# Kernel optimization log

Hardware: AMD Instinct MI355X
Metric: run time of the kernel (lower is better)

## Reference

```python
import jax, jax.numpy as jnp
import numpy as np

EPS = 1e-7
IOU_THRESHOLD = 0.5
PENALTY_FACTOR = 0.1
BOX_LOSS_WEIGHT = 5.0
OBJ_LOSS_WEIGHT = 1.0
SMALL_OBJ_SCALE = 2.0
SMALL_SIZE_THRESHOLD = 0.05


def _xywh_to_xyxy(b):
    return jnp.concatenate([b[..., :2] - b[..., 2:] / 2, b[..., :2] + b[..., 2:] / 2], axis=-1)


def _bbox_ciou(box1, box2, eps=EPS):
    # box1, box2: (..., 4) in xyxy format
    b1_x1, b1_y1, b1_x2, b1_y2 = box1[..., 0], box1[..., 1], box1[..., 2], box1[..., 3]
    b2_x1, b2_y1, b2_x2, b2_y2 = box2[..., 0], box2[..., 1], box2[..., 2], box2[..., 3]
    b1_area = (b1_x2 - b1_x1) * (b1_y2 - b1_y1)
    b2_area = (b2_x2 - b2_x1) * (b2_y2 - b2_y1)
    inter_w = jnp.clip(jnp.minimum(b1_x2, b2_x2) - jnp.maximum(b1_x1, b2_x1), 0)
    inter_h = jnp.clip(jnp.minimum(b1_y2, b2_y2) - jnp.maximum(b1_y1, b2_y1), 0)
    inter_area = inter_w * inter_h
    union_area = b1_area + b2_area - inter_area + eps
    iou = inter_area / union_area
    c2 = (jnp.maximum(b1_x2, b2_x2) - jnp.minimum(b1_x1, b2_x1)) ** 2 + \
         (jnp.maximum(b1_y2, b2_y2) - jnp.minimum(b1_y1, b2_y1)) ** 2 + eps
    center_dist2 = ((b1_x1 + b1_x2) / 2 - (b2_x1 + b2_x2) / 2) ** 2 + \
                   ((b1_y1 + b1_y2) / 2 - (b2_y1 + b2_y2) / 2) ** 2
    w1, h1 = b1_x2 - b1_x1, b1_y2 - b1_y1
    w2, h2 = b2_x2 - b2_x1, b2_y2 - b2_y1
    v = (4.0 / (jnp.pi ** 2)) * (jnp.arctan(w1 / (h1 + eps)) - jnp.arctan(w2 / (h2 + eps))) ** 2
    alpha = v / (1 - iou + v + eps)
    return iou - (center_dist2 / c2 + alpha * v)


def setup_inputs() -> dict:
    key = jax.random.key(0)
    k0, k1, k2, k3, k4 = jax.random.split(key, 5)
    B, Np, Ng, C = 16, 8192, 128, 80
    return {
        "batch_y_hat": jax.random.uniform(k0, (B, Np, 4), dtype=jnp.float32),
        "batch_y": jax.random.uniform(k1, (B, Ng, 4), dtype=jnp.float32),
        "batch_obj_scores": jax.random.normal(k2, (B, Np), dtype=jnp.float32),
        "batch_class_pred": jax.random.normal(k3, (B, Np, C), dtype=jnp.float32),
        "batch_class_target": jax.random.randint(k4, (B, Ng), 0, C),
        "min_obj_score": 0,
    }


def reference(batch_y_hat, batch_y, batch_obj_scores, batch_class_pred, batch_class_target, min_obj_score):
    valid = batch_obj_scores > min_obj_score                      # (B, Np) kept predictions
    p = _xywh_to_xyxy(batch_y_hat)                                # (B, Np, 4)
    g = _xywh_to_xyxy(batch_y)                                    # (B, Ng, 4)
    # pairwise IoU (xywh compute_iou, which has no eps)
    lt = jnp.maximum(p[:, :, None, :2], g[:, None, :, :2])       # (B, Np, Ng, 2)
    rb = jnp.minimum(p[:, :, None, 2:], g[:, None, :, 2:])
    wh = jnp.clip(rb - lt, 0)
    inter = wh[..., 0] * wh[..., 1]                               # (B, Np, Ng)
    area_p = (p[..., 2] - p[..., 0]) * (p[..., 3] - p[..., 1])
    area_g = (g[..., 2] - g[..., 0]) * (g[..., 3] - g[..., 1])
    iou_mat = inter / (area_p[:, :, None] + area_g[:, None, :] - inter)
    max_iou = jnp.max(iou_mat, axis=-1)                           # (B, Np)
    match_idx = jnp.argmax(iou_mat, axis=-1)                      # (B, Np)
    matched = valid & (max_iou > IOU_THRESHOLD)
    unmatched = valid & ~matched
    # CIoU localization loss over matched preds
    matched_gt_xyxy = jnp.take_along_axis(g, match_idx[..., None], axis=1)   # (B, Np, 4)
    ciou_loss = 1.0 - _bbox_ciou(p, matched_gt_xyxy)              # (B, Np)
    is_small = (batch_y[..., 2] < SMALL_SIZE_THRESHOLD) | (batch_y[..., 3] < SMALL_SIZE_THRESHOLD)  # (B, Ng)
    w_small = jnp.where(jnp.take_along_axis(is_small, match_idx, axis=1), SMALL_OBJ_SCALE, 1.0)
    n_match = jnp.sum(matched, axis=1)
    loc_loss = jnp.where(n_match > 0,
                         jnp.sum(ciou_loss * w_small * matched, axis=1) / jnp.maximum(n_match, 1),
                         0.0)
    # classification loss over matched preds
    logp = jax.nn.log_softmax(batch_class_pred, axis=-1)          # (B, Np, C)
    tgt = jnp.take_along_axis(batch_class_target, match_idx, axis=1)
    ce = -jnp.take_along_axis(logp, tgt[..., None], axis=-1)[..., 0]
    cls_loss = jnp.where(n_match > 0,
                         jnp.sum(ce * w_small * matched, axis=1) / jnp.maximum(n_match, 1),
                         0.0)
    # penalty on unmatched objectness scores
    penalty = PENALTY_FACTOR * jnp.sum(batch_obj_scores * unmatched, axis=1)
    # objectness BCE-with-logits over valid preds, FN reweighted x2
    s = batch_obj_scores
    lbl = matched.astype(s.dtype)
    bce = jnp.clip(s, 0) - s * lbl + jnp.log1p(jnp.exp(-jnp.abs(s)))
    w_obj = jnp.where(matched & (s < 0.5), 2.0, 1.0)
    n_valid = jnp.sum(valid, axis=1)
    obj_loss = jnp.where(n_valid > 0,
                         jnp.sum(bce * w_obj * valid, axis=1) / jnp.maximum(n_valid, 1),
                         0.0)
    per_batch = BOX_LOSS_WEIGHT * loc_loss + OBJ_LOSS_WEIGHT * obj_loss + penalty + cls_loss
    valid_b = n_valid > 0
    n_vb = jnp.sum(valid_b)
    return jnp.sum(jnp.where(valid_b, per_batch, 0.0)) / jnp.maximum(n_vb, 1)
```

## Files before the change

kernel.cpp:

```cpp
#include <hip/hip_runtime.h>
#include <math.h>

#define B_  16
#define NP_ 8192
#define NG_ 128
#define NC_ 80

#define EPS_       1e-7f
#define IOU_THR_   0.5f
#define PEN_       0.1f
#define BOXW_      5.0f
#define SMALLSC_   2.0f
#define SMALLTH_   0.05f


__global__ __launch_bounds__(256) void yolo_main(
    const float* __restrict__ y_hat,
    const float* __restrict__ ygt,
    const float* __restrict__ obj,
    const float* __restrict__ clsp,
    const int*   __restrict__ tgt,
    const int*   __restrict__ min_s,
    float* __restrict__ acc)
{
    __shared__ float gx1[NG_], gy1[NG_], gx2[NG_], gy2[NG_], garea[NG_], gws[NG_];
    __shared__ int   gtc[NG_];
    __shared__ float wred[4][6];

    const int b   = blockIdx.y;
    const int tid = threadIdx.x;
    const int p   = blockIdx.x * 256 + tid;

    if (tid < NG_) {
        float4 gb = *(const float4*)(ygt + ((size_t)b * NG_ + tid) * 4);
        float x1 = gb.x - gb.z * 0.5f, y1 = gb.y - gb.w * 0.5f;
        float x2 = gb.x + gb.z * 0.5f, y2 = gb.y + gb.w * 0.5f;
        gx1[tid] = x1; gy1[tid] = y1; gx2[tid] = x2; gy2[tid] = y2;
        garea[tid] = (x2 - x1) * (y2 - y1);
        gws[tid]   = ((gb.z < SMALLTH_) || (gb.w < SMALLTH_)) ? SMALLSC_ : 1.0f;
        gtc[tid]   = tgt[b * NG_ + tid];
    }
    __syncthreads();

    const float min_score = (float)min_s[0];

    float4 pb = *(const float4*)(y_hat + ((size_t)b * NP_ + p) * 4);
    float px1 = pb.x - pb.z * 0.5f, py1 = pb.y - pb.w * 0.5f;
    float px2 = pb.x + pb.z * 0.5f, py2 = pb.y + pb.w * 0.5f;
    float area_p = (px2 - px1) * (py2 - py1);

    float bi_inter = -1.0f, bi_union = 1.0f;
    int   bi = 0;
    #pragma unroll 8
    for (int j = 0; j < NG_; ++j) {
        float ltx = fmaxf(px1, gx1[j]);
        float lty = fmaxf(py1, gy1[j]);
        float rbx = fminf(px2, gx2[j]);
        float rby = fminf(py2, gy2[j]);
        float w = fmaxf(rbx - ltx, 0.0f);
        float h = fmaxf(rby - lty, 0.0f);
        float inter = w * h;
        float uni = area_p + garea[j] - inter;
        bool better = inter * bi_union > bi_inter * uni;
        bi_inter = better ? inter : bi_inter;
        bi_union = better ? uni   : bi_union;
        bi       = better ? j     : bi;
    }
    float max_iou = bi_inter / bi_union;

    float s = obj[(size_t)b * NP_ + p];
    bool valid     = s > min_score;
    bool matched   = valid && (max_iou > IOU_THR_);
    bool unmatched = valid && !matched;

    float f_loc = 0.f, f_ce = 0.f, f_pen = 0.f, f_bce = 0.f;
    float n_m = matched ? 1.f : 0.f;
    float n_v = valid   ? 1.f : 0.f;

    if (unmatched) f_pen = PEN_ * s;

    if (valid) {
        float lbl = matched ? 1.f : 0.f;
        float bce = fmaxf(s, 0.f) - s * lbl + log1pf(expf(-fabsf(s)));
        float w_obj = (matched && s < 0.5f) ? 2.f : 1.f;
        f_bce = bce * w_obj;
    }

    if (matched) {
        float wsm = gws[bi];
        float bx1 = gx1[bi], by1 = gy1[bi], bx2 = gx2[bi], by2 = gy2[bi];
        float b1a = (px2 - px1) * (py2 - py1);
        float b2a = (bx2 - bx1) * (by2 - by1);
        float iw = fmaxf(fminf(px2, bx2) - fmaxf(px1, bx1), 0.f);
        float ih = fmaxf(fminf(py2, by2) - fmaxf(py1, by1), 0.f);
        float inter = iw * ih;
        float uni = b1a + b2a - inter + EPS_;
        float iou = inter / uni;
        float cw = fmaxf(px2, bx2) - fminf(px1, bx1);
        float ch = fmaxf(py2, by2) - fminf(py1, by1);
        float c2 = cw * cw + ch * ch + EPS_;
        float dx = (px1 + px2) * 0.5f - (bx1 + bx2) * 0.5f;
        float dy = (py1 + py2) * 0.5f - (by1 + by2) * 0.5f;
        float rho2 = dx * dx + dy * dy;
        float w1 = px2 - px1, h1 = py2 - py1;
        float w2 = bx2 - bx1, h2 = by2 - by1;
        float dat = atanf(w1 / (h1 + EPS_)) - atanf(w2 / (h2 + EPS_));
        float v = (float)(4.0 / (M_PI * M_PI)) * dat * dat;
        float alpha = v / (1.f - iou + v + EPS_);
        float ciou = iou - (rho2 / c2 + alpha * v);
        f_loc = (1.f - ciou) * wsm;

        const float* row = clsp + ((size_t)b * NP_ + p) * NC_;
        float m = -INFINITY;
        #pragma unroll
        for (int k = 0; k < NC_ / 4; ++k) {
            float4 v4 = ((const float4*)row)[k];
            m = fmaxf(m, fmaxf(fmaxf(v4.x, v4.y), fmaxf(v4.z, v4.w)));
        }
        float se = 0.f;
        #pragma unroll
        for (int k = 0; k < NC_ / 4; ++k) {
            float4 v4 = ((const float4*)row)[k];
            se += expf(v4.x - m) + expf(v4.y - m) + expf(v4.z - m) + expf(v4.w - m);
        }
        int t = gtc[bi];
        float ce = -(row[t] - m - logf(se));
        f_ce = ce * wsm;
    }

    float vals[6] = { n_m, n_v, f_loc, f_ce, f_pen, f_bce };
    #pragma unroll
    for (int i = 0; i < 6; ++i) {
        float v = vals[i];
        #pragma unroll
        for (int off = 32; off > 0; off >>= 1)
            v += __shfl_down(v, off, 64);
        vals[i] = v;
    }
    int wave = tid >> 6, lane = tid & 63;
    if (lane == 0) {
        #pragma unroll
        for (int i = 0; i < 6; ++i) wred[wave][i] = vals[i];
    }
    __syncthreads();
    if (tid == 0) {
        #pragma unroll
        for (int i = 0; i < 6; ++i) {
            float v = wred[0][i] + wred[1][i] + wred[2][i] + wred[3][i];
            atomicAdd(&acc[b * 6 + i], v);
        }
    }
}

__global__ __launch_bounds__(64) void yolo_final(const float* __restrict__ acc,
                                                 float* __restrict__ out)
{
    int b = threadIdx.x;
    float pb = 0.f, cnt = 0.f;
    if (b < B_) {
        float nm   = acc[b * 6 + 0];
        float nv   = acc[b * 6 + 1];
        float sloc = acc[b * 6 + 2];
        float sce  = acc[b * 6 + 3];
        float spen = acc[b * 6 + 4];
        float sbce = acc[b * 6 + 5];
        float loc = nm > 0.f ? sloc / nm : 0.f;
        float ce  = nm > 0.f ? sce  / nm : 0.f;
        float ob  = nv > 0.f ? sbce / nv : 0.f;
        float per = BOXW_ * loc + ob + spen + ce;
        if (nv > 0.f) { pb = per; cnt = 1.f; }
    }
    #pragma unroll
    for (int off = 32; off > 0; off >>= 1) {
        pb  += __shfl_down(pb,  off, 64);
        cnt += __shfl_down(cnt, off, 64);
    }
    if (b == 0) out[0] = pb / fmaxf(cnt, 1.f);
}

extern "C" void kernel_launch(void* const* d_in, const int* in_sizes, int n_in,
                              void* d_out, int out_size, void* d_ws, size_t ws_size,
                              hipStream_t stream) {
    const float* y_hat = (const float*)d_in[0];
    const float* ygt   = (const float*)d_in[1];
    const float* obj   = (const float*)d_in[2];
    const float* clsp  = (const float*)d_in[3];
    const int*   tgt   = (const int*)d_in[4];
    const int*   mins  = (const int*)d_in[5];
    float* acc = (float*)d_ws;
    float* out = (float*)d_out;

    hipMemsetAsync(acc, 0, B_ * 6 * sizeof(float), stream);

    dim3 grid(NP_ / 256, B_);
    yolo_main<<<grid, 256, 0, stream>>>(y_hat, ygt, obj, clsp, tgt, mins, acc);
    yolo_final<<<1, 64, 0, stream>>>(acc, out);
}
```

Measured before the change: 115.2 us.

## Split GT matching across two thread halves and drop atomics for per-block partials

Each block now handles 128 predictions with 256 threads: each half scans 64 ground-truth boxes and the two argmax results are merged through shared memory. This doubles the grid and shortens the serial IoU loop per thread. Block sums go to a per-block partial buffer instead of atomics, which removes the memset, and the final kernel reduces those partials. GT boxes are stored as float4 in shared memory. The cost is an extra barrier, and half the threads sit idle during the loss tail.

```diff
diff --git a/kernel.cpp b/kernel.cpp
--- a/kernel.cpp
+++ b/kernel.cpp
@@ -5,6 +5,8 @@
 #define NP_ 8192
 #define NG_ 128
 #define NC_ 80
+#define PPB_ 128
+#define NBX_ (NP_ / PPB_)
 
 #define EPS_       1e-7f
 #define IOU_THR_   0.5f
@@ -21,21 +23,25 @@
     const float* __restrict__ clsp,
     const int*   __restrict__ tgt,
     const int*   __restrict__ min_s,
-    float* __restrict__ acc)
+    float* __restrict__ part)
 {
-    __shared__ float gx1[NG_], gy1[NG_], gx2[NG_], gy2[NG_], garea[NG_], gws[NG_];
-    __shared__ int   gtc[NG_];
-    __shared__ float wred[4][6];
-
-    const int b   = blockIdx.y;
-    const int tid = threadIdx.x;
-    const int p   = blockIdx.x * 256 + tid;
+    __shared__ float4 g4[NG_];
+    __shared__ float  garea[NG_], gws[NG_];
+    __shared__ int    gtc[NG_];
+    __shared__ float  mbuf[PPB_][4];
+    __shared__ float  wred[4][6];
+
+    const int b    = blockIdx.y;
+    const int tid  = threadIdx.x;
+    const int pl   = tid & (PPB_ - 1);
+    const int half = tid >> 7;
+    const int p    = blockIdx.x * PPB_ + pl;
 
     if (tid < NG_) {
         float4 gb = *(const float4*)(ygt + ((size_t)b * NG_ + tid) * 4);
         float x1 = gb.x - gb.z * 0.5f, y1 = gb.y - gb.w * 0.5f;
         float x2 = gb.x + gb.z * 0.5f, y2 = gb.y + gb.w * 0.5f;
-        gx1[tid] = x1; gy1[tid] = y1; gx2[tid] = x2; gy2[tid] = y2;
+        g4[tid] = make_float4(x1, y1, x2, y2);
         garea[tid] = (x2 - x1) * (y2 - y1);
         gws[tid]   = ((gb.z < SMALLTH_) || (gb.w < SMALLTH_)) ? SMALLSC_ : 1.0f;
         gtc[tid]   = tgt[b * NG_ + tid];
@@ -50,15 +56,14 @@
     float area_p = (px2 - px1) * (py2 - py1);
 
     float bi_inter = -1.0f, bi_union = 1.0f;
-    int   bi = 0;
+    int   bi = half * 64;
+    const int j0 = half * 64;
     #pragma unroll 8
-    for (int j = 0; j < NG_; ++j) {
-        float ltx = fmaxf(px1, gx1[j]);
-        float lty = fmaxf(py1, gy1[j]);
-        float rbx = fminf(px2, gx2[j]);
-        float rby = fminf(py2, gy2[j]);
-        float w = fmaxf(rbx - ltx, 0.0f);
-        float h = fmaxf(rby - lty, 0.0f);
+    for (int jj = 0; jj < 64; ++jj) {
+        int j = j0 + jj;
+        float4 g = g4[j];
+        float w = fmaxf(fminf(px2, g.z) - fmaxf(px1, g.x), 0.0f);
+        float h = fmaxf(fminf(py2, g.w) - fmaxf(py1, g.y), 0.0f);
         float inter = w * h;
         float uni = area_p + garea[j] - inter;
         bool better = inter * bi_union > bi_inter * uni;
@@ -66,66 +71,81 @@
         bi_union = better ? uni   : bi_union;
         bi       = better ? j     : bi;
     }
-    float max_iou = bi_inter / bi_union;
-
-    float s = obj[(size_t)b * NP_ + p];
-    bool valid     = s > min_score;
-    bool matched   = valid && (max_iou > IOU_THR_);
-    bool unmatched = valid && !matched;
-
-    float f_loc = 0.f, f_ce = 0.f, f_pen = 0.f, f_bce = 0.f;
-    float n_m = matched ? 1.f : 0.f;
-    float n_v = valid   ? 1.f : 0.f;
-
-    if (unmatched) f_pen = PEN_ * s;
-
-    if (valid) {
-        float lbl = matched ? 1.f : 0.f;
-        float bce = fmaxf(s, 0.f) - s * lbl + log1pf(expf(-fabsf(s)));
-        float w_obj = (matched && s < 0.5f) ? 2.f : 1.f;
-        f_bce = bce * w_obj;
-    }
-
-    if (matched) {
-        float wsm = gws[bi];
-        float bx1 = gx1[bi], by1 = gy1[bi], bx2 = gx2[bi], by2 = gy2[bi];
-        float b1a = (px2 - px1) * (py2 - py1);
-        float b2a = (bx2 - bx1) * (by2 - by1);
-        float iw = fmaxf(fminf(px2, bx2) - fmaxf(px1, bx1), 0.f);
-        float ih = fmaxf(fminf(py2, by2) - fmaxf(py1, by1), 0.f);
-        float inter = iw * ih;
-        float uni = b1a + b2a - inter + EPS_;
-        float iou = inter / uni;
-        float cw = fmaxf(px2, bx2) - fminf(px1, bx1);
-        float ch = fmaxf(py2, by2) - fminf(py1, by1);
-        float c2 = cw * cw + ch * ch + EPS_;
-        float dx = (px1 + px2) * 0.5f - (bx1 + bx2) * 0.5f;
-        float dy = (py1 + py2) * 0.5f - (by1 + by2) * 0.5f;
-        float rho2 = dx * dx + dy * dy;
-        float w1 = px2 - px1, h1 = py2 - py1;
-        float w2 = bx2 - bx1, h2 = by2 - by1;
-        float dat = atanf(w1 / (h1 + EPS_)) - atanf(w2 / (h2 + EPS_));
-        float v = (float)(4.0 / (M_PI * M_PI)) * dat * dat;
-        float alpha = v / (1.f - iou + v + EPS_);
-        float ciou = iou - (rho2 / c2 + alpha * v);
-        f_loc = (1.f - ciou) * wsm;
-
-        const float* row = clsp + ((size_t)b * NP_ + p) * NC_;
-        float m = -INFINITY;
-        #pragma unroll
-        for (int k = 0; k < NC_ / 4; ++k) {
-            float4 v4 = ((const float4*)row)[k];
-            m = fmaxf(m, fmaxf(fmaxf(v4.x, v4.y), fmaxf(v4.z, v4.w)));
+
+    if (half == 1) {
+        mbuf[pl][0] = bi_inter;
+        mbuf[pl][1] = bi_union;
+        mbuf[pl][2] = (float)bi;
+    }
+    __syncthreads();
+
+    float f_loc = 0.f, f_ce = 0.f, f_pen = 0.f, f_bce = 0.f, n_m = 0.f, n_v = 0.f;
+
+    if (half == 0) {
+        float oi = mbuf[pl][0], ou = mbuf[pl][1];
+        if (oi * bi_union > bi_inter * ou) {
+            bi_inter = oi; bi_union = ou; bi = (int)mbuf[pl][2];
         }
-        float se = 0.f;
-        #pragma unroll
-        for (int k = 0; k < NC_ / 4; ++k) {
-            float4 v4 = ((const float4*)row)[k];
-            se += expf(v4.x - m) + expf(v4.y - m) + expf(v4.z - m) + expf(v4.w - m);
+        float max_iou = bi_inter / bi_union;
+
+        float s = obj[(size_t)b * NP_ + p];
+        bool valid     = s > min_score;
+        bool matched   = valid && (max_iou > IOU_THR_);
+        bool unmatched = valid && !matched;
+
+        n_m = matched ? 1.f : 0.f;
+        n_v = valid   ? 1.f : 0.f;
+        if (unmatched) f_pen = PEN_ * s;
+
+        if (valid) {
+            float lbl = matched ? 1.f : 0.f;
+            float bce = fmaxf(s, 0.f) - s * lbl + log1pf(expf(-fabsf(s)));
+            float w_obj = (matched && s < 0.5f) ? 2.f : 1.f;
+            f_bce = bce * w_obj;
         }
-        int t = gtc[bi];
-        float ce = -(row[t] - m - logf(se));
-        f_ce = ce * wsm;
+
+        if (matched) {
+            float wsm = gws[bi];
+            float4 g = g4[bi];
+            float bx1 = g.x, by1 = g.y, bx2 = g.z, by2 = g.w;
+            float b1a = (px2 - px1) * (py2 - py1);
+            float b2a = (bx2 - bx1) * (by2 - by1);
+            float iw = fmaxf(fminf(px2, bx2) - fmaxf(px1, bx1), 0.f);
+            float ih = fmaxf(fminf(py2, by2) - fmaxf(py1, by1), 0.f);
+            float inter = iw * ih;
+            float uni = b1a + b2a - inter + EPS_;
+            float iou = inter / uni;
+            float cw = fmaxf(px2, bx2) - fminf(px1, bx1);
+            float ch = fmaxf(py2, by2) - fminf(py1, by1);
+            float c2 = cw * cw + ch * ch + EPS_;
+            float dx = (px1 + px2) * 0.5f - (bx1 + bx2) * 0.5f;
+            float dy = (py1 + py2) * 0.5f - (by1 + by2) * 0.5f;
+            float rho2 = dx * dx + dy * dy;
+            float w1 = px2 - px1, h1 = py2 - py1;
+            float w2 = bx2 - bx1, h2 = by2 - by1;
+            float dat = atanf(w1 / (h1 + EPS_)) - atanf(w2 / (h2 + EPS_));
+            float v = (float)(4.0 / (M_PI * M_PI)) * dat * dat;
+            float alpha = v / (1.f - iou + v + EPS_);
+            float ciou = iou - (rho2 / c2 + alpha * v);
+            f_loc = (1.f - ciou) * wsm;
+
+            const float* row = clsp + ((size_t)b * NP_ + p) * NC_;
+            float m = -INFINITY;
+            #pragma unroll
+            for (int k = 0; k < NC_ / 4; ++k) {
+                float4 v4 = ((const float4*)row)[k];
+                m = fmaxf(m, fmaxf(fmaxf(v4.x, v4.y), fmaxf(v4.z, v4.w)));
+            }
+            float se = 0.f;
+            #pragma unroll
+            for (int k = 0; k < NC_ / 4; ++k) {
+                float4 v4 = ((const float4*)row)[k];
+                se += expf(v4.x - m) + expf(v4.y - m) + expf(v4.z - m) + expf(v4.w - m);
+            }
+            int t = gtc[bi];
+            float ce = -(row[t] - m - logf(se));
+            f_ce = ce * wsm;
+        }
     }
 
     float vals[6] = { n_m, n_v, f_loc, f_ce, f_pen, f_bce };
@@ -144,38 +164,47 @@
     }
     __syncthreads();
     if (tid == 0) {
-        #pragma unroll
-        for (int i = 0; i < 6; ++i) {
-            float v = wred[0][i] + wred[1][i] + wred[2][i] + wred[3][i];
-            atomicAdd(&acc[b * 6 + i], v);
-        }
+        float* slot = part + ((size_t)b * NBX_ + blockIdx.x) * 6;
+        #pragma unroll
+        for (int i = 0; i < 6; ++i)
+            slot[i] = wred[0][i] + wred[1][i] + wred[2][i] + wred[3][i];
     }
 }
 
-__global__ __launch_bounds__(64) void yolo_final(const float* __restrict__ acc,
+__global__ __launch_bounds__(64) void yolo_final(const float* __restrict__ part,
                                                  float* __restrict__ out)
 {
-    int b = threadIdx.x;
-    float pb = 0.f, cnt = 0.f;
-    if (b < B_) {
-        float nm   = acc[b * 6 + 0];
-        float nv   = acc[b * 6 + 1];
-        float sloc = acc[b * 6 + 2];
-        float sce  = acc[b * 6 + 3];
-        float spen = acc[b * 6 + 4];
-        float sbce = acc[b * 6 + 5];
-        float loc = nm > 0.f ? sloc / nm : 0.f;
-        float ce  = nm > 0.f ? sce  / nm : 0.f;
-        float ob  = nv > 0.f ? sbce / nv : 0.f;
-        float per = BOXW_ * loc + ob + spen + ce;
-        if (nv > 0.f) { pb = per; cnt = 1.f; }
+    int lane = threadIdx.x;
+    int b    = lane >> 2;
+    int sub  = lane & 3;
+
+    float v[6] = {0.f, 0.f, 0.f, 0.f, 0.f, 0.f};
+    for (int k = 0; k < NBX_ / 4; ++k) {
+        const float* slot = part + ((size_t)b * NBX_ + sub + 4 * k) * 6;
+        #pragma unroll
+        for (int i = 0; i < 6; ++i) v[i] += slot[i];
+    }
+    #pragma unroll
+    for (int i = 0; i < 6; ++i) {
+        v[i] += __shfl_xor(v[i], 1, 64);
+        v[i] += __shfl_xor(v[i], 2, 64);
+    }
+
+    float pbv = 0.f, cnt = 0.f;
+    if (sub == 0) {
+        float nm = v[0], nv = v[1];
+        float loc = nm > 0.f ? v[2] / nm : 0.f;
+        float ce  = nm > 0.f ? v[3] / nm : 0.f;
+        float ob  = nv > 0.f ? v[5] / nv : 0.f;
+        float per = BOXW_ * loc + ob + v[4] + ce;
+        if (nv > 0.f) { pbv = per; cnt = 1.f; }
     }
     #pragma unroll
     for (int off = 32; off > 0; off >>= 1) {
-        pb  += __shfl_down(pb,  off, 64);
+        pbv += __shfl_down(pbv, off, 64);
         cnt += __shfl_down(cnt, off, 64);
     }
-    if (b == 0) out[0] = pb / fmaxf(cnt, 1.f);
+    if (lane == 0) out[0] = pbv / fmaxf(cnt, 1.f);
 }
 
 extern "C" void kernel_launch(void* const* d_in, const int* in_sizes, int n_in,
@@ -187,12 +216,10 @@
     const float* clsp  = (const float*)d_in[3];
     const int*   tgt   = (const int*)d_in[4];
     const int*   mins  = (const int*)d_in[5];
-    float* acc = (float*)d_ws;
-    float* out = (float*)d_out;
-
-    hipMemsetAsync(acc, 0, B_ * 6 * sizeof(float), stream);
-
-    dim3 grid(NP_ / 256, B_);
-    yolo_main<<<grid, 256, 0, stream>>>(y_hat, ygt, obj, clsp, tgt, mins, acc);
-    yolo_final<<<1, 64, 0, stream>>>(acc, out);
+    float* part = (float*)d_ws;
+    float* out  = (float*)d_out;
+
+    dim3 grid(NBX_, B_);
+    yolo_main<<<grid, 256, 0, stream>>>(y_hat, ygt, obj, clsp, tgt, mins, part);
+    yolo_final<<<1, 64, 0, stream>>>(part, out);
 }
```

Measured after the change: 106.0 us. 8.0% less time.
